# Performance work log

Measured on AMD Instinct MI355X. Metric: run time of the kernel, lower is better.

The kernel has to match this reference:

```python
import jax, jax.numpy as jnp
import numpy as np

B, N, M = 32, 65536, 64
IMG = 640.0
POS_THR, NEG_THR = 0.5, 0.4
ALPHA, GAMMA = 0.25, 2.0
BBOX_W = 2.0
EPS = 1e-6


def setup_inputs() -> dict:
    key = jax.random.key(0)
    k1, k2, k3, k4, k5 = jax.random.split(key, 5)
    # predictions: cx, cy in [0, IMG], w, h in [8, 72], obj logit ~ N(0,1)
    cxcy = jax.random.uniform(k1, (B, N, 2), jnp.float32) * IMG
    wh = jax.random.uniform(k2, (B, N, 2), jnp.float32) * 64.0 + 8.0
    obj = jax.random.normal(k3, (B, N, 1), jnp.float32)
    predictions = jnp.concatenate([cxcy, wh, obj], axis=-1)  # [B, N, 5]
    # ground-truth boxes in xyxy, centers in [0, IMG], sizes in [10, 100]
    gcxcy = jax.random.uniform(k4, (B, M, 2), jnp.float32) * IMG
    gwh = jax.random.uniform(k5, (B, M, 2), jnp.float32) * 90.0 + 10.0
    gt_boxes = jnp.concatenate([gcxcy - gwh / 2, gcxcy + gwh / 2], axis=-1)  # [B, M, 4]
    return {"predictions": predictions, "gt_boxes": gt_boxes}


def _focal(logits, targets):
    # stable BCE-with-logits, then focal modulation
    bce = jnp.maximum(logits, 0.0) - logits * targets + jnp.log1p(jnp.exp(-jnp.abs(logits)))
    p = jax.nn.sigmoid(logits)
    p_t = jnp.where(targets == 1.0, p, 1.0 - p)
    alpha_t = jnp.where(targets == 1.0, ALPHA, 1.0 - ALPHA)
    return alpha_t * (1.0 - p_t) ** GAMMA * bce


def _pairwise_iou(pb, gb):
    # pb: [N,4] xyxy, gb: [M,4] xyxy -> [N,M]
    x1 = jnp.maximum(pb[:, None, 0], gb[None, :, 0])
    y1 = jnp.maximum(pb[:, None, 1], gb[None, :, 1])
    x2 = jnp.minimum(pb[:, None, 2], gb[None, :, 2])
    y2 = jnp.minimum(pb[:, None, 3], gb[None, :, 3])
    inter = jnp.clip(x2 - x1, 0.0) * jnp.clip(y2 - y1, 0.0)
    area_p = (pb[:, 2] - pb[:, 0]) * (pb[:, 3] - pb[:, 1])
    area_g = (gb[:, 2] - gb[:, 0]) * (gb[:, 3] - gb[:, 1])
    union = area_p[:, None] + area_g[None, :] - inter
    return inter / jnp.clip(union, EPS)


def _giou_term(pb, gb):
    # elementwise 1 - GIoU; pb, gb: [N,4]
    x1 = jnp.maximum(pb[:, 0], gb[:, 0]); y1 = jnp.maximum(pb[:, 1], gb[:, 1])
    x2 = jnp.minimum(pb[:, 2], gb[:, 2]); y2 = jnp.minimum(pb[:, 3], gb[:, 3])
    inter = jnp.clip(x2 - x1, 0.0) * jnp.clip(y2 - y1, 0.0)
    area_p = (pb[:, 2] - pb[:, 0]) * (pb[:, 3] - pb[:, 1])
    area_g = (gb[:, 2] - gb[:, 0]) * (gb[:, 3] - gb[:, 1])
    union = area_p + area_g - inter
    iou = inter / jnp.clip(union, EPS)
    ex1 = jnp.minimum(pb[:, 0], gb[:, 0]); ey1 = jnp.minimum(pb[:, 1], gb[:, 1])
    ex2 = jnp.maximum(pb[:, 2], gb[:, 2]); ey2 = jnp.maximum(pb[:, 3], gb[:, 3])
    enc = (ex2 - ex1) * (ey2 - ey1)
    giou = iou - (enc - union) / jnp.clip(enc, EPS)
    return 1.0 - giou


def _per_image(pred, gt):
    # pred: [N,5] (cx,cy,w,h,obj), gt: [M,4] xyxy
    cx, cy, w, h = pred[:, 0], pred[:, 1], pred[:, 2], pred[:, 3]
    pb = jnp.stack([cx - w / 2, cy - h / 2, cx + w / 2, cy + h / 2], axis=1)  # decode to xyxy
    obj = pred[:, 4]
    ious = _pairwise_iou(pb, gt)  # [N, M]
    best_pred_per_gt = ious.max(axis=0)              # [M]
    best_pred_idx = jnp.argmax(ious, axis=0)         # [M]
    best_gt_per_pred = ious.max(axis=1)              # [N]
    best_gt_idx = jnp.argmax(ious, axis=1)           # [N]
    # force-match each GT's best anchor if its IoU > 0.1 (scatter-max)
    pos_scatter = jnp.zeros((pred.shape[0],), jnp.int32).at[best_pred_idx].max(
        (best_pred_per_gt > 0.1).astype(jnp.int32))
    pos = (pos_scatter > 0) | (best_gt_per_pred > POS_THR)
    neg = best_gt_per_pred < NEG_THR
    valid = pos | neg
    t = pos.astype(jnp.float32)
    fl = _focal(obj, t)
    vcnt = valid.sum().astype(jnp.float32)
    cls_loss = jnp.where(vcnt > 0, (fl * valid).sum() / jnp.maximum(vcnt, 1.0), 0.0)
    matched = gt[best_gt_idx]                        # [N,4]
    gterm = _giou_term(pb, matched)                  # [N]
    pcnt = pos.sum().astype(jnp.float32)
    reg_loss = jnp.where(pcnt > 0, (gterm * pos).sum() / jnp.maximum(pcnt, 1.0), 0.0)
    return cls_loss, reg_loss, pos.sum()


def reference(predictions, gt_boxes):
    cls_b, reg_b, npos_b = jax.vmap(_per_image)(predictions, gt_boxes)
    num_pos = jnp.maximum(npos_b.sum(), 1).astype(jnp.float32)
    bsz = jnp.float32(predictions.shape[0])
    total_cls = cls_b.sum() / bsz
    total_reg = reg_b.sum() / num_pos * bsz
    return total_cls + BBOX_W * total_reg
```

## Files before the change

kernel.cpp:

```cpp
#include <hip/hip_runtime.h>

#define NB 32
#define NPRED 65536
#define NGT 64
#define BLK 256
#define SLICES 64
#define PPT 4
#define NXB 32
#define BIN_SCALE 0.05f

#define POS_THR 0.5f
#define NEG_THR 0.4f
#define SCAT_THR 0.1f
#define EPSF 1e-6f


__device__ __forceinline__ int binidx(float x) {
    int bi = (int)(x * BIN_SCALE);
    return max(0, min(NXB - 1, bi));
}

__device__ __forceinline__ float focal_shared(float l, bool pos) {
    float e  = expf(-fabsf(l));
    float lg = log1pf(e);
    float rp = 1.f / (1.f + e);
    float p  = (l >= 0.f) ? rp : (1.f - rp);
    if (pos) { float q = 1.f - p; return 0.25f * q * q * ((fmaxf(l, 0.f) - l) + lg); }
    return 0.75f * p * p * (fmaxf(l, 0.f) + lg);
}

__device__ __forceinline__ float giou_term(float px1, float py1, float px2, float py2,
                                           float gx1, float gy1, float gx2, float gy2) {
    float x1 = fmaxf(px1, gx1), y1 = fmaxf(py1, gy1);
    float x2 = fminf(px2, gx2), y2 = fminf(py2, gy2);
    float dx = fmaxf(__fsub_rn(x2, x1), 0.f);
    float dy = fmaxf(__fsub_rn(y2, y1), 0.f);
    float inter = __fmul_rn(dx, dy);
    float ap = __fmul_rn(__fsub_rn(px2, px1), __fsub_rn(py2, py1));
    float ag = __fmul_rn(__fsub_rn(gx2, gx1), __fsub_rn(gy2, gy1));
    float uni = __fsub_rn(__fadd_rn(ap, ag), inter);
    float iou = __fdiv_rn(inter, fmaxf(uni, EPSF));
    float ex1 = fminf(px1, gx1), ey1 = fminf(py1, gy1);
    float ex2 = fmaxf(px2, gx2), ey2 = fmaxf(py2, gy2);
    float enc = __fmul_rn(__fsub_rn(ex2, ex1), __fsub_rn(ey2, ey1));
    float giou = __fsub_rn(iou, __fdiv_rn(__fsub_rn(enc, uni), fmaxf(enc, EPSF)));
    return __fsub_rn(1.f, giou);
}


__global__ __launch_bounds__(BLK) void passA(
    const float* __restrict__ pred, const float* __restrict__ gt,
    unsigned long long* __restrict__ keys,
    double* __restrict__ S_fl, double* __restrict__ S_gt,
    int* __restrict__ vcnt, int* __restrict__ pcnt)
{
    const int b = blockIdx.y;
    const int slice = blockIdx.x;
    const int tid = threadIdx.x;

    __shared__ float sgx1[NGT], sgy1[NGT], sgx2[NGT], sgy2[NGT], sgar[NGT];
    __shared__ unsigned long long skey[NGT];
    __shared__ unsigned long long binx[NXB], biny[NXB];
    __shared__ float rfl[BLK / 64], rgt[BLK / 64];
    __shared__ int rvp[BLK / 64];

    const unsigned base_n = (unsigned)(slice * (BLK * PPT));
    const float4* src4 = (const float4*)(pred + (size_t)b * NPRED * 5 + (size_t)base_n * 5)
                         + (size_t)tid * 5;
    float4 q0 = src4[0], q1 = src4[1], q2 = src4[2], q3 = src4[3], q4 = src4[4];

    const float4* gtb = (const float4*)(gt + (size_t)b * NGT * 4);
    float4 gmine;
    if (tid < NGT) gmine = gtb[tid];
    if (tid < NXB) { binx[tid] = 0ULL; biny[tid] = 0ULL; }
    if (tid < NGT) {
        sgx1[tid] = gmine.x; sgy1[tid] = gmine.y;
        sgx2[tid] = gmine.z; sgy2[tid] = gmine.w;
        sgar[tid] = __fmul_rn(__fsub_rn(gmine.z, gmine.x), __fsub_rn(gmine.w, gmine.y));
        skey[tid] = 0ULL;
    }
    __syncthreads();
    if (tid < NGT) {
        unsigned long long bit = 1ULL << tid;
        int b1 = binidx(gmine.x), b2 = binidx(gmine.z);
        #pragma unroll
        for (int i = 0; i < 6; ++i) { int bb = min(b1 + i, NXB - 1); if (b1 + i <= b2) atomicOr(&binx[bb], bit); }
        b1 = binidx(gmine.y); b2 = binidx(gmine.w);
        #pragma unroll
        for (int i = 0; i < 6; ++i) { int bb = min(b1 + i, NXB - 1); if (b1 + i <= b2) atomicOr(&biny[bb], bit); }
    }
    __syncthreads();

    const float cxa[PPT] = {q0.x, q1.y, q2.z, q3.w};
    const float cya[PPT] = {q0.y, q1.z, q2.w, q4.x};
    const float wa [PPT] = {q0.z, q1.w, q3.x, q4.y};
    const float ha [PPT] = {q0.w, q2.x, q3.y, q4.z};
    const float oba[PPT] = {q1.x, q2.y, q3.z, q4.w};

    float acc_fl = 0.f, acc_gt = 0.f;
    int acc_vp = 0;

    #pragma unroll
    for (int i = 0; i < PPT; ++i) {
        const float px1 = __fsub_rn(cxa[i], __fmul_rn(wa[i], 0.5f));
        const float py1 = __fsub_rn(cya[i], __fmul_rn(ha[i], 0.5f));
        const float px2 = __fadd_rn(cxa[i], __fmul_rn(wa[i], 0.5f));
        const float py2 = __fadd_rn(cya[i], __fmul_rn(ha[i], 0.5f));
        const float area_p = __fmul_rn(__fsub_rn(px2, px1), __fsub_rn(py2, py1));

        unsigned long long mx = 0ULL, my = 0ULL;
        {
            int b1 = binidx(px1), b2 = binidx(px2);
            #pragma unroll
            for (int k = 0; k < 5; ++k) { unsigned long long v = binx[min(b1 + k, NXB - 1)]; if (b1 + k <= b2) mx |= v; }
            b1 = binidx(py1); b2 = binidx(py2);
            #pragma unroll
            for (int k = 0; k < 5; ++k) { unsigned long long v = biny[min(b1 + k, NXB - 1)]; if (b1 + k <= b2) my |= v; }
        }
        unsigned long long m = mx & my;

        const unsigned n = base_n + (unsigned)(PPT * tid + i);
        const unsigned long long nkey = (unsigned long long)(~n);

        float best_iou = 0.f;
        int best_j = 0;
        while (m) {
            int j0 = __ffsll(m) - 1; m &= m - 1;
            int j1 = -1;
            if (m) { j1 = __ffsll(m) - 1; m &= m - 1; }
            int j1c = (j1 >= 0) ? j1 : j0;
            float ax1 = sgx1[j0], ay1 = sgy1[j0], ax2 = sgx2[j0], ay2 = sgy2[j0], aga = sgar[j0];
            float bx1 = sgx1[j1c], by1 = sgy1[j1c], bx2 = sgx2[j1c], by2 = sgy2[j1c], agb = sgar[j1c];
            {
                float x1 = fmaxf(px1, ax1), y1 = fmaxf(py1, ay1);
                float x2 = fminf(px2, ax2), y2 = fminf(py2, ay2);
                float dx = fmaxf(__fsub_rn(x2, x1), 0.f);
                float dy = fmaxf(__fsub_rn(y2, y1), 0.f);
                float inter = __fmul_rn(dx, dy);
                if (inter > 0.f) {
                    float uni = __fsub_rn(__fadd_rn(area_p, aga), inter);
                    float iou = __fdiv_rn(inter, fmaxf(uni, EPSF));
                    if (iou > best_iou) { best_iou = iou; best_j = j0; }
                    if (iou > SCAT_THR)
                        atomicMax(&skey[j0], (((unsigned long long)__float_as_uint(iou)) << 32) | nkey);
                }
            }
            if (j1 >= 0) {
                float x1 = fmaxf(px1, bx1), y1 = fmaxf(py1, by1);
                float x2 = fminf(px2, bx2), y2 = fminf(py2, by2);
                float dx = fmaxf(__fsub_rn(x2, x1), 0.f);
                float dy = fmaxf(__fsub_rn(y2, y1), 0.f);
                float inter = __fmul_rn(dx, dy);
                if (inter > 0.f) {
                    float uni = __fsub_rn(__fadd_rn(area_p, agb), inter);
                    float iou = __fdiv_rn(inter, fmaxf(uni, EPSF));
                    if (iou > best_iou) { best_iou = iou; best_j = j1; }
                    if (iou > SCAT_THR)
                        atomicMax(&skey[j1], (((unsigned long long)__float_as_uint(iou)) << 32) | nkey);
                }
            }
        }

        const bool pos0   = best_iou > POS_THR;
        const bool negf   = best_iou < NEG_THR;
        const bool valid0 = pos0 || negf;
        if (valid0) acc_fl += focal_shared(oba[i], pos0);
        if (pos0) {
            acc_gt += giou_term(px1, py1, px2, py2,
                                sgx1[best_j], sgy1[best_j], sgx2[best_j], sgy2[best_j]);
        }
        acc_vp += (valid0 ? 1 : 0) | (pos0 ? 0x10000 : 0);
    }

    for (int off = 32; off; off >>= 1) {
        acc_fl += __shfl_down(acc_fl, off);
        acc_gt += __shfl_down(acc_gt, off);
        acc_vp += __shfl_down(acc_vp, off);
    }
    int wid = tid >> 6;
    if ((tid & 63) == 0) { rfl[wid] = acc_fl; rgt[wid] = acc_gt; rvp[wid] = acc_vp; }
    __syncthreads();
    if (tid == 0) {
        float sfl = 0.f, sgt2 = 0.f; int svp = 0;
        #pragma unroll
        for (int i = 0; i < BLK / 64; ++i) { sfl += rfl[i]; sgt2 += rgt[i]; svp += rvp[i]; }
        atomicAdd(&S_fl[b], (double)sfl);
        atomicAdd(&S_gt[b], (double)sgt2);
        atomicAdd(&vcnt[b], svp & 0xFFFF);
        atomicAdd(&pcnt[b], svp >> 16);
    }
    if (tid < NGT) {
        unsigned long long k = skey[tid];
        if (k) atomicMax(&keys[b * NGT + tid], k);
    }
}


__global__ __launch_bounds__(64) void passBC(
    const float* __restrict__ pred, const float* __restrict__ gt,
    const unsigned long long* __restrict__ keys,
    const double* __restrict__ S_fl, const double* __restrict__ S_gt,
    const int* __restrict__ vcnt, const int* __restrict__ pcnt,
    float* __restrict__ cls_b, float* __restrict__ reg_b, int* __restrict__ npos_b,
    unsigned* __restrict__ done, float* __restrict__ out)
{
    const int b = blockIdx.x;
    const int lane = threadIdx.x;

    __shared__ float4 sgt[NGT];
    __shared__ unsigned cn_list[NGT];

    const float4* gtb = (const float4*)(gt + (size_t)b * NGT * 4);
    float4 gj = gtb[lane];
    sgt[lane] = gj;

    unsigned long long key = keys[b * NGT + lane];
    float miou = __uint_as_float((unsigned)(key >> 32));
    unsigned n = ~((unsigned)(key & 0xFFFFFFFFULL));
    bool qual = miou > SCAT_THR;

    bool unique = qual;
    for (int j2 = 0; j2 < NGT; ++j2) {
        unsigned bn = __shfl(n, j2);
        int bq = __shfl((int)qual, j2);
        if (bq && j2 < lane && bn == n) unique = false;
    }
    unsigned long long mask = __ballot(unique ? 1 : 0);
    int NC = __popcll(mask);
    int slot = __popcll(mask & ((1ULL << lane) - 1ULL));
    if (unique) cn_list[slot] = n;
    __syncthreads();

    float cx = 0.f, cy = 0.f, w = 0.f, h = 0.f, obj = 0.f;
    if (lane < NC) {
        const float* p = pred + (size_t)b * NPRED * 5 + (size_t)cn_list[lane] * 5;
        cx = p[0]; cy = p[1]; w = p[2]; h = p[3]; obj = p[4];
    }
    float px1 = __fsub_rn(cx, __fmul_rn(w, 0.5f));
    float py1 = __fsub_rn(cy, __fmul_rn(h, 0.5f));
    float px2 = __fadd_rn(cx, __fmul_rn(w, 0.5f));
    float py2 = __fadd_rn(cy, __fmul_rn(h, 0.5f));
    float area_p = __fmul_rn(__fsub_rn(px2, px1), __fsub_rn(py2, py1));

    float bv = 0.f; int bj = 0;
    #pragma unroll 4
    for (int j = 0; j < NGT; ++j) {
        float4 g = sgt[j];
        float x1 = fmaxf(px1, g.x), y1 = fmaxf(py1, g.y);
        float x2 = fminf(px2, g.z), y2 = fminf(py2, g.w);
        float dx = fmaxf(__fsub_rn(x2, x1), 0.f);
        float dy = fmaxf(__fsub_rn(y2, y1), 0.f);
        float inter = __fmul_rn(dx, dy);
        if (inter > 0.f) {
            float ag = __fmul_rn(__fsub_rn(g.z, g.x), __fsub_rn(g.w, g.y));
            float uni = __fsub_rn(__fadd_rn(area_p, ag), inter);
            float iou = __fdiv_rn(inter, fmaxf(uni, EPSF));
            if (iou > bv) { bv = iou; bj = j; }
        }
    }

    double add_fl = 0.0, add_gt = 0.0;
    int add_v = 0, add_p = 0;
    if (lane < NC && !(bv > POS_THR)) {
        bool was_neg = bv < NEG_THR;
        float f1 = focal_shared(obj, true);
        float f0 = focal_shared(obj, false);
        add_fl = (double)f1 - (was_neg ? (double)f0 : 0.0);
        add_v = was_neg ? 0 : 1;
        add_p = 1;
        float4 gb = sgt[bj];
        add_gt = (double)giou_term(px1, py1, px2, py2, gb.x, gb.y, gb.z, gb.w);
    }

    for (int off = 32; off; off >>= 1) {
        add_fl += __shfl_down(add_fl, off);
        add_gt += __shfl_down(add_gt, off);
        add_v  += __shfl_down(add_v, off);
        add_p  += __shfl_down(add_p, off);
    }

    if (lane == 0) {
        double sfl = S_fl[b] + add_fl;
        double sgt2 = S_gt[b] + add_gt;
        int v = vcnt[b] + add_v;
        int pc = pcnt[b] + add_p;
        cls_b[b] = (v > 0) ? (float)(sfl / (double)(v > 1 ? v : 1)) : 0.f;
        reg_b[b] = (pc > 0) ? (float)(sgt2 / (double)(pc > 1 ? pc : 1)) : 0.f;
        npos_b[b] = pc;
    }

    __threadfence();
    unsigned t = 0;
    if (lane == 0) t = atomicAdd(done, 1u);
    t = __shfl(t, 0);
    if (t == NB - 1) {
        __threadfence();
        volatile float* vc = cls_b;
        volatile float* vr = reg_b;
        volatile int*   vn = npos_b;
        float cv = (lane < NB) ? vc[lane] : 0.f;
        float rv = (lane < NB) ? vr[lane] : 0.f;
        int   nv = (lane < NB) ? vn[lane] : 0;
        for (int off = 32; off; off >>= 1) {
            cv += __shfl_down(cv, off);
            rv += __shfl_down(rv, off);
            nv += __shfl_down(nv, off);
        }
        if (lane == 0) {
            float num_pos = fmaxf((float)nv, 1.f);
            out[0] = cv / (float)NB + 2.0f * (rv / num_pos * (float)NB);
        }
    }
}


extern "C" void kernel_launch(void* const* d_in, const int* in_sizes, int n_in,
                              void* d_out, int out_size, void* d_ws, size_t ws_size,
                              hipStream_t stream) {
    const float* pred = (const float*)d_in[0];
    const float* gt   = (const float*)d_in[1];
    float* out = (float*)d_out;

    char* ws = (char*)d_ws;
    unsigned long long* keys = (unsigned long long*)(ws + 0);
    double* S_fl   = (double*)(ws + 16384);
    double* S_gt   = (double*)(ws + 16640);
    int* vcnt      = (int*)(ws + 16896);
    int* pcnt      = (int*)(ws + 17024);
    float* cls_b   = (float*)(ws + 17152);
    float* reg_b   = (float*)(ws + 17280);
    int* npos_b    = (int*)(ws + 17408);
    unsigned* done = (unsigned*)(ws + 17536);

    hipMemsetAsync(d_ws, 0, 17664, stream);

    dim3 gridA(SLICES, NB);
    passA<<<gridA, BLK, 0, stream>>>(pred, gt, keys, S_fl, S_gt, vcnt, pcnt);
    passBC<<<NB, 64, 0, stream>>>(pred, gt, keys, S_fl, S_gt, vcnt, pcnt,
                                  cls_b, reg_b, npos_b, done, out);
}
```

Before: 123.6 us.

## Replace coarse bin bitmasks with prefix/suffix cumulative masks for candidate GT lookup

Replaces the 32-bin x/y occupancy bitmasks, which needed up to ten shared loads per prediction, with 128-bin cumulative OR masks built by wave-level prefix and suffix scans. Each prediction now gets its candidate GT set from four shared loads and three ANDs, and the finer bins should admit fewer false candidates. The first two candidates are also evaluated branch-free, using a zero-filled sentinel GT slot, before the general loop. The cost is extra setup per block (scans, more shared memory) and some wasted work when a prediction has fewer than two candidates.

```diff
diff --git a/kernel.cpp b/kernel.cpp
--- a/kernel.cpp
+++ b/kernel.cpp
@@ -6,8 +6,8 @@
 #define BLK 256
 #define SLICES 64
 #define PPT 4
-#define NXB 32
-#define BIN_SCALE 0.05f
+#define NCB 128
+#define CBIN_SCALE 0.2f
 
 #define POS_THR 0.5f
 #define NEG_THR 0.4f
@@ -15,9 +15,9 @@
 #define EPSF 1e-6f
 
 
-__device__ __forceinline__ int binidx(float x) {
-    int bi = (int)(x * BIN_SCALE);
-    return max(0, min(NXB - 1, bi));
+__device__ __forceinline__ int cbin(float x) {
+    int bi = (int)(x * CBIN_SCALE);
+    return max(0, min(NCB - 1, bi));
 }
 
 __device__ __forceinline__ float focal_shared(float l, bool pos) {
@@ -57,10 +57,12 @@
     const int b = blockIdx.y;
     const int slice = blockIdx.x;
     const int tid = threadIdx.x;
-
-    __shared__ float sgx1[NGT], sgy1[NGT], sgx2[NGT], sgy2[NGT], sgar[NGT];
+    const int lane = tid & 63;
+    const int wv = tid >> 6;
+
+    __shared__ float sgx1[NGT + 1], sgy1[NGT + 1], sgx2[NGT + 1], sgy2[NGT + 1], sgar[NGT + 1];
     __shared__ unsigned long long skey[NGT];
-    __shared__ unsigned long long binx[NXB], biny[NXB];
+    __shared__ unsigned long long cums[4][NCB];
     __shared__ float rfl[BLK / 64], rgt[BLK / 64];
     __shared__ int rvp[BLK / 64];
 
@@ -72,22 +74,52 @@
     const float4* gtb = (const float4*)(gt + (size_t)b * NGT * 4);
     float4 gmine;
     if (tid < NGT) gmine = gtb[tid];
-    if (tid < NXB) { binx[tid] = 0ULL; biny[tid] = 0ULL; }
+    ((unsigned long long*)cums)[tid] = 0ULL;
+    ((unsigned long long*)cums)[tid + BLK] = 0ULL;
     if (tid < NGT) {
         sgx1[tid] = gmine.x; sgy1[tid] = gmine.y;
         sgx2[tid] = gmine.z; sgy2[tid] = gmine.w;
         sgar[tid] = __fmul_rn(__fsub_rn(gmine.z, gmine.x), __fsub_rn(gmine.w, gmine.y));
         skey[tid] = 0ULL;
-    }
-    __syncthreads();
+    } else if (tid == NGT) {
+        sgx1[NGT] = 0.f; sgy1[NGT] = 0.f; sgx2[NGT] = 0.f; sgy2[NGT] = 0.f; sgar[NGT] = 0.f;
+    }
+    __syncthreads();
+
     if (tid < NGT) {
         unsigned long long bit = 1ULL << tid;
-        int b1 = binidx(gmine.x), b2 = binidx(gmine.z);
-        #pragma unroll
-        for (int i = 0; i < 6; ++i) { int bb = min(b1 + i, NXB - 1); if (b1 + i <= b2) atomicOr(&binx[bb], bit); }
-        b1 = binidx(gmine.y); b2 = binidx(gmine.w);
-        #pragma unroll
-        for (int i = 0; i < 6; ++i) { int bb = min(b1 + i, NXB - 1); if (b1 + i <= b2) atomicOr(&biny[bb], bit); }
+        atomicOr(&cums[0][cbin(gmine.x)], bit);
+        atomicOr(&cums[1][cbin(gmine.z)], bit);
+        atomicOr(&cums[2][cbin(gmine.y)], bit);
+        atomicOr(&cums[3][cbin(gmine.w)], bit);
+    }
+    __syncthreads();
+
+    {
+        unsigned long long v0 = cums[wv][2 * lane];
+        unsigned long long v1 = cums[wv][2 * lane + 1];
+        unsigned long long v = v0 | v1;
+        if ((wv & 1) == 0) {
+            #pragma unroll
+            for (int off = 1; off < 64; off <<= 1) {
+                unsigned long long t = __shfl_up(v, off);
+                if (lane >= off) v |= t;
+            }
+            unsigned long long prev = __shfl_up(v, 1);
+            if (lane == 0) prev = 0ULL;
+            cums[wv][2 * lane]     = prev | v0;
+            cums[wv][2 * lane + 1] = v;
+        } else {
+            #pragma unroll
+            for (int off = 1; off < 64; off <<= 1) {
+                unsigned long long t = __shfl_down(v, off);
+                if (lane + off < 64) v |= t;
+            }
+            unsigned long long nxt = __shfl_down(v, 1);
+            if (lane == 63) nxt = 0ULL;
+            cums[wv][2 * lane]     = v;
+            cums[wv][2 * lane + 1] = v1 | nxt;
+        }
     }
     __syncthreads();
 
@@ -108,29 +140,53 @@
         const float py2 = __fadd_rn(cya[i], __fmul_rn(ha[i], 0.5f));
         const float area_p = __fmul_rn(__fsub_rn(px2, px1), __fsub_rn(py2, py1));
 
-        unsigned long long mx = 0ULL, my = 0ULL;
-        {
-            int b1 = binidx(px1), b2 = binidx(px2);
-            #pragma unroll
-            for (int k = 0; k < 5; ++k) { unsigned long long v = binx[min(b1 + k, NXB - 1)]; if (b1 + k <= b2) mx |= v; }
-            b1 = binidx(py1); b2 = binidx(py2);
-            #pragma unroll
-            for (int k = 0; k < 5; ++k) { unsigned long long v = biny[min(b1 + k, NXB - 1)]; if (b1 + k <= b2) my |= v; }
-        }
-        unsigned long long m = mx & my;
+        unsigned long long m = (cums[1][cbin(px1)] & cums[0][cbin(px2)])
+                             & (cums[3][cbin(py1)] & cums[2][cbin(py2)]);
 
         const unsigned n = base_n + (unsigned)(PPT * tid + i);
         const unsigned long long nkey = (unsigned long long)(~n);
 
         float best_iou = 0.f;
         int best_j = 0;
+
+        int j0 = NGT, j1 = NGT;
+        if (m) { j0 = __ffsll(m) - 1; m &= m - 1; }
+        if (m) { j1 = __ffsll(m) - 1; m &= m - 1; }
+        {
+            float ax1 = sgx1[j0], ay1 = sgy1[j0], ax2 = sgx2[j0], ay2 = sgy2[j0], aga = sgar[j0];
+            float bx1 = sgx1[j1], by1 = sgy1[j1], bx2 = sgx2[j1], by2 = sgy2[j1], agb = sgar[j1];
+            float x1 = fmaxf(px1, ax1), y1 = fmaxf(py1, ay1);
+            float x2 = fminf(px2, ax2), y2 = fminf(py2, ay2);
+            float dx = fmaxf(__fsub_rn(x2, x1), 0.f);
+            float dy = fmaxf(__fsub_rn(y2, y1), 0.f);
+            float inter = __fmul_rn(dx, dy);
+            float uni = __fsub_rn(__fadd_rn(area_p, aga), inter);
+            float iou = __fdiv_rn(inter, fmaxf(uni, EPSF));
+            iou = (inter > 0.f) ? iou : 0.f;
+            if (iou > best_iou) { best_iou = iou; best_j = j0; }
+            if (iou > SCAT_THR)
+                atomicMax(&skey[j0], (((unsigned long long)__float_as_uint(iou)) << 32) | nkey);
+
+            float X1 = fmaxf(px1, bx1), Y1 = fmaxf(py1, by1);
+            float X2 = fminf(px2, bx2), Y2 = fminf(py2, by2);
+            float dX = fmaxf(__fsub_rn(X2, X1), 0.f);
+            float dY = fmaxf(__fsub_rn(Y2, Y1), 0.f);
+            float interB = __fmul_rn(dX, dY);
+            float uniB = __fsub_rn(__fadd_rn(area_p, agb), interB);
+            float iouB = __fdiv_rn(interB, fmaxf(uniB, EPSF));
+            iouB = (interB > 0.f) ? iouB : 0.f;
+            if (iouB > best_iou) { best_iou = iouB; best_j = j1; }
+            if (iouB > SCAT_THR)
+                atomicMax(&skey[j1], (((unsigned long long)__float_as_uint(iouB)) << 32) | nkey);
+        }
+
         while (m) {
-            int j0 = __ffsll(m) - 1; m &= m - 1;
-            int j1 = -1;
-            if (m) { j1 = __ffsll(m) - 1; m &= m - 1; }
-            int j1c = (j1 >= 0) ? j1 : j0;
-            float ax1 = sgx1[j0], ay1 = sgy1[j0], ax2 = sgx2[j0], ay2 = sgy2[j0], aga = sgar[j0];
-            float bx1 = sgx1[j1c], by1 = sgy1[j1c], bx2 = sgx2[j1c], by2 = sgy2[j1c], agb = sgar[j1c];
+            int ja = __ffsll(m) - 1; m &= m - 1;
+            int jb = -1;
+            if (m) { jb = __ffsll(m) - 1; m &= m - 1; }
+            int jbc = (jb >= 0) ? jb : NGT;
+            float ax1 = sgx1[ja], ay1 = sgy1[ja], ax2 = sgx2[ja], ay2 = sgy2[ja], aga = sgar[ja];
+            float bx1 = sgx1[jbc], by1 = sgy1[jbc], bx2 = sgx2[jbc], by2 = sgy2[jbc], agb = sgar[jbc];
             {
                 float x1 = fmaxf(px1, ax1), y1 = fmaxf(py1, ay1);
                 float x2 = fminf(px2, ax2), y2 = fminf(py2, ay2);
@@ -140,12 +196,12 @@
                 if (inter > 0.f) {
                     float uni = __fsub_rn(__fadd_rn(area_p, aga), inter);
                     float iou = __fdiv_rn(inter, fmaxf(uni, EPSF));
-                    if (iou > best_iou) { best_iou = iou; best_j = j0; }
+                    if (iou > best_iou) { best_iou = iou; best_j = ja; }
                     if (iou > SCAT_THR)
-                        atomicMax(&skey[j0], (((unsigned long long)__float_as_uint(iou)) << 32) | nkey);
+                        atomicMax(&skey[ja], (((unsigned long long)__float_as_uint(iou)) << 32) | nkey);
                 }
             }
-            if (j1 >= 0) {
+            if (jb >= 0) {
                 float x1 = fmaxf(px1, bx1), y1 = fmaxf(py1, by1);
                 float x2 = fminf(px2, bx2), y2 = fminf(py2, by2);
                 float dx = fmaxf(__fsub_rn(x2, x1), 0.f);
@@ -154,9 +210,9 @@
                 if (inter > 0.f) {
                     float uni = __fsub_rn(__fadd_rn(area_p, agb), inter);
                     float iou = __fdiv_rn(inter, fmaxf(uni, EPSF));
-                    if (iou > best_iou) { best_iou = iou; best_j = j1; }
+                    if (iou > best_iou) { best_iou = iou; best_j = jb; }
                     if (iou > SCAT_THR)
-                        atomicMax(&skey[j1], (((unsigned long long)__float_as_uint(iou)) << 32) | nkey);
+                        atomicMax(&skey[jb], (((unsigned long long)__float_as_uint(iou)) << 32) | nkey);
                 }
             }
         }
@@ -177,8 +233,7 @@
         acc_gt += __shfl_down(acc_gt, off);
         acc_vp += __shfl_down(acc_vp, off);
     }
-    int wid = tid >> 6;
-    if ((tid & 63) == 0) { rfl[wid] = acc_fl; rgt[wid] = acc_gt; rvp[wid] = acc_vp; }
+    if (lane == 0) { rfl[wv] = acc_fl; rgt[wv] = acc_gt; rvp[wv] = acc_vp; }
     __syncthreads();
     if (tid == 0) {
         float sfl = 0.f, sgt2 = 0.f; int svp = 0;
```

Measured after the change: 121.0 us, median of 2. 1.02x faster.
